# Kernel optimization log

Measured on AMD Instinct MI355X. Metric: run time of the kernel, lower is better.

The kernel has to match this reference:

```python
import jax, jax.numpy as jnp
import numpy as np

B, S, D, H = 4, 2048, 1024, 16
HD = D // H


def setup_inputs() -> dict:
    key = jax.random.key(0)
    ks = jax.random.split(key, 6)
    s = 1.0 / np.sqrt(D)
    return {
        "x": jax.random.normal(ks[0], (B, S, D), dtype=jnp.float32),
        "Wq": jax.random.normal(ks[1], (D, D), dtype=jnp.float32) * s,
        "Wk": jax.random.normal(ks[2], (D, D), dtype=jnp.float32) * s,
        "Wv": jax.random.normal(ks[3], (D, D), dtype=jnp.float32) * s,
        "Wo": jax.random.normal(ks[4], (D, D), dtype=jnp.float32) * s,
        "bo": jnp.zeros((D,), dtype=jnp.float32),
    }


def reference(x, Wq, Wk, Wv, Wo, bo):
    b, n, d = x.shape
    # QKV projections (torch Linear: x @ W.T, but weights here are stored as [d_in, d_out])
    q = (x @ Wq).reshape(b, n, H, HD).transpose(0, 2, 1, 3)  # [b,h,n,hd]
    k = (x @ Wk).reshape(b, n, H, HD).transpose(0, 2, 1, 3)
    v = (x @ Wv).reshape(b, n, H, HD).transpose(0, 2, 1, 3)
    scores = jnp.einsum("bhqd,bhkd->bhqk", q, k) / np.sqrt(HD)
    causal = jnp.tril(jnp.ones((n, n), dtype=bool))  # True = keep
    scores = jnp.where(causal, scores, -jnp.inf)
    attn = jax.nn.softmax(scores, axis=-1)
    ctx = jnp.einsum("bhqk,bhkd->bhqd", attn, v)
    ctx = ctx.transpose(0, 2, 1, 3).reshape(b, n, d)
    return ctx @ Wo + bo
```

## Files before the change

kernel.cpp:

```cpp
#include <hip/hip_runtime.h>
#include <hip/hip_bf16.h>

typedef __bf16 bf16;
typedef __bf16 bf16x4 __attribute__((ext_vector_type(4)));
typedef __bf16 bf16x8 __attribute__((ext_vector_type(8)));
typedef float f32x4 __attribute__((ext_vector_type(4)));

static constexpr int Bn = 4, Sn = 2048, Dn = 1024, Hn = 16, HDn = 64;
static constexpr int Mn = Bn * Sn;

__device__ __forceinline__ void gload_lds16(const void* g, void* l) {
  __builtin_amdgcn_global_load_lds(
      (const __attribute__((address_space(1))) unsigned int*)g,
      (__attribute__((address_space(3))) unsigned int*)l, 16, 0, 0);
}

__global__ void cvt_x_kernel(const float* __restrict__ x, bf16* __restrict__ xb, int n8) {
  int i = blockIdx.x * blockDim.x + threadIdx.x;
  if (i >= n8) return;
  const float4* p = reinterpret_cast<const float4*>(x) + (size_t)i * 2;
  float4 a = p[0], b = p[1];
  bf16x8 v;
  v[0] = (bf16)a.x; v[1] = (bf16)a.y; v[2] = (bf16)a.z; v[3] = (bf16)a.w;
  v[4] = (bf16)b.x; v[5] = (bf16)b.y; v[6] = (bf16)b.z; v[7] = (bf16)b.w;
  *(reinterpret_cast<bf16x8*>(xb) + i) = v;
}

struct alignas(8) B4 { bf16 e[4]; };

__global__ void transpose_w_kernel(const float* __restrict__ W0, const float* __restrict__ W1,
                                   const float* __restrict__ W2, const float* __restrict__ W3,
                                   bf16* __restrict__ WtQKV, bf16* __restrict__ Wot) {
  __shared__ bf16 tile[64][65];
  const int which = blockIdx.z;
  const float* W = (which == 0) ? W0 : (which == 1) ? W1 : (which == 2) ? W2 : W3;
  bf16* out = (which < 3) ? (WtQKV + (size_t)which * 1024 * 1024) : Wot;
  const int k0 = blockIdx.y * 64, n0 = blockIdx.x * 64;
  const int t = threadIdx.x;
  const int tr = t >> 4, tc = (t & 15) * 4;
#pragma unroll
  for (int rr = 0; rr < 4; ++rr) {
    const int row = rr * 16 + tr;
    float4 v = *reinterpret_cast<const float4*>(&W[(size_t)(k0 + row) * 1024 + n0 + tc]);
    tile[row][tc + 0] = (bf16)v.x; tile[row][tc + 1] = (bf16)v.y;
    tile[row][tc + 2] = (bf16)v.z; tile[row][tc + 3] = (bf16)v.w;
  }
  __syncthreads();
#pragma unroll
  for (int rr = 0; rr < 4; ++rr) {
    const int row = rr * 16 + tr;
    B4 o;
#pragma unroll
    for (int j = 0; j < 4; ++j) o.e[j] = tile[tc + j][row];
    *reinterpret_cast<B4*>(&out[(size_t)(n0 + row) * 1024 + k0 + tc]) = o;
  }
}

template <int MODE>
__global__ __launch_bounds__(256, 2)
void gemm_kernel(const bf16* __restrict__ A, const bf16* __restrict__ Bt,
                 float* __restrict__ Co, const float* __restrict__ bias,
                 bf16* __restrict__ Qo, bf16* __restrict__ Ko, bf16* __restrict__ Vto) {
  __shared__ bf16 Al[2][128 * 64];
  __shared__ bf16 Bl[2][128 * 64];
  const int tid = threadIdx.x;
  const int lane = tid & 63;
  const int wv = tid >> 6;
  const int wm = wv >> 1, wn = wv & 1;
  const int lr = lane & 15, lg = lane >> 4;
  const int m0 = blockIdx.y * 128, n0 = blockIdx.x * 128;

  int soff[4];
  const bf16* srcA[4];
  const bf16* srcB[4];
#pragma unroll
  for (int it = 0; it < 4; ++it) {
    const int elem = it * 2048 + tid * 8;
    const int row = elem >> 6;
    const int g = (elem >> 3) & 7;
    const int gs = g ^ (row & 7);
    soff[it] = elem;
    srcA[it] = A + (size_t)(m0 + row) * 1024 + gs * 8;
    srcB[it] = Bt + (size_t)(n0 + row) * 1024 + gs * 8;
  }

  f32x4 acc[4][4] = {};

#pragma unroll
  for (int it = 0; it < 4; ++it) {
    gload_lds16(srcA[it], (bf16*)&Al[0][0] + soff[it]);
    gload_lds16(srcB[it], (bf16*)&Bl[0][0] + soff[it]);
  }
  __syncthreads();

  for (int ks = 0; ks < 16; ++ks) {
    const int cur = ks & 1;
    if (ks + 1 < 16) {
      const int kn = (ks + 1) * 64;
#pragma unroll
      for (int it = 0; it < 4; ++it) {
        gload_lds16(srcA[it] + kn, (bf16*)&Al[cur ^ 1][0] + soff[it]);
        gload_lds16(srcB[it] + kn, (bf16*)&Bl[cur ^ 1][0] + soff[it]);
      }
    }
    const bf16* AlF = Al[cur];
    const bf16* BlF = Bl[cur];
#pragma unroll
    for (int kk = 0; kk < 2; ++kk) {
      bf16x8 af[4], bfr[4];
#pragma unroll
      for (int i = 0; i < 4; ++i) {
        const int row = wm * 64 + i * 16 + lr;
        af[i] = *reinterpret_cast<const bf16x8*>(AlF + row * 64 + (((kk * 4 + lg) ^ (row & 7)) << 3));
      }
#pragma unroll
      for (int i = 0; i < 4; ++i) {
        const int row = wn * 64 + i * 16 + lr;
        bfr[i] = *reinterpret_cast<const bf16x8*>(BlF + row * 64 + (((kk * 4 + lg) ^ (row & 7)) << 3));
      }
#pragma unroll
      for (int mi = 0; mi < 4; ++mi)
#pragma unroll
        for (int ni = 0; ni < 4; ++ni)
          acc[mi][ni] = __builtin_amdgcn_mfma_f32_16x16x32_bf16(af[mi], bfr[ni], acc[mi][ni], 0, 0, 0);
    }
    __syncthreads();
  }

  const int mrow = lg * 4;
  if (MODE == 0) {
    const int w = n0 >> 10;
    const int nl0 = n0 & 1023;
    if (w == 2) {
      const int b = m0 >> 11;
      const int s0 = (m0 & 2047) + wm * 64 + mrow;
#pragma unroll
      for (int ni = 0; ni < 4; ++ni) {
        const int nl = nl0 + wn * 64 + ni * 16 + lr;
        const int h = nl >> 6, hd = nl & 63;
        bf16* vbase = Vto + ((size_t)(b * 16 + h) * 64 + hd) * 2048;
#pragma unroll
        for (int mi = 0; mi < 4; ++mi) {
          B4 o;
#pragma unroll
          for (int i = 0; i < 4; ++i) o.e[i] = (bf16)acc[mi][ni][i];
          *reinterpret_cast<B4*>(&vbase[s0 + mi * 16]) = o;
        }
      }
    } else {
      const float fs = (w == 0) ? 0.18033688011112042f : 1.0f;
#pragma unroll
      for (int ni = 0; ni < 4; ++ni) {
        const int nl = nl0 + wn * 64 + ni * 16 + lr;
        const int h = nl >> 6, hd = nl & 63;
        bf16* dst = (w == 0) ? Qo : Ko;
#pragma unroll
        for (int mi = 0; mi < 4; ++mi) {
#pragma unroll
          for (int i = 0; i < 4; ++i) {
            const int m_g = m0 + wm * 64 + mi * 16 + mrow + i;
            const int b = m_g >> 11, s = m_g & 2047;
            dst[((size_t)(b * 16 + h) * 2048 + s) * 64 + hd] = (bf16)(acc[mi][ni][i] * fs);
          }
        }
      }
    }
  } else {
#pragma unroll
    for (int ni = 0; ni < 4; ++ni) {
      const int n_g = n0 + wn * 64 + ni * 16 + lr;
      const float bv = bias[n_g];
#pragma unroll
      for (int mi = 0; mi < 4; ++mi) {
#pragma unroll
        for (int i = 0; i < 4; ++i) {
          const int m_g = m0 + wm * 64 + mi * 16 + mrow + i;
          Co[(size_t)m_g * 1024 + n_g] = acc[mi][ni][i] + bv;
        }
      }
    }
  }
}

__device__ __forceinline__ unsigned int pack2(float lo, float hi) {
  union { bf16 bb[2]; unsigned int u; } c;
  c.bb[0] = (bf16)lo; c.bb[1] = (bf16)hi;
  return c.u;
}

__device__ __forceinline__ void attn_tile(const bf16* __restrict__ KlF,
                                          const bf16* __restrict__ VlF,
                                          const bf16x8 (&aq)[2], f32x4 (&acc)[4],
                                          float& lst, int kv0, int qrow, bool domask,
                                          int lr, int lg) {
  f32x4 sc[4] = {};
#pragma unroll
  for (int kk = 0; kk < 2; ++kk) {
    bf16x8 ak[4];
#pragma unroll
    for (int ni = 0; ni < 4; ++ni) {
      const int row = ni * 16 + lr;
      ak[ni] = *reinterpret_cast<const bf16x8*>(KlF + row * 64 + (((kk * 4 + lg) ^ (row & 7)) << 3));
    }
    __builtin_amdgcn_s_setprio(1);
#pragma unroll
    for (int ni = 0; ni < 4; ++ni)
      sc[ni] = __builtin_amdgcn_mfma_f32_16x16x32_bf16(ak[ni], aq[kk], sc[ni], 0, 0, 0);
    __builtin_amdgcn_s_setprio(0);
  }
  float p[4][4];
  float rs = 0.f;
#pragma unroll
  for (int ni = 0; ni < 4; ++ni)
#pragma unroll
    for (int r = 0; r < 4; ++r) {
      float pv = __builtin_amdgcn_exp2f(sc[ni][r]);
      if (domask && (kv0 + ni * 16 + lg * 4 + r > qrow)) pv = 0.f;
      p[ni][r] = pv;
      rs += pv;
    }
  rs += __shfl_xor(rs, 16);
  rs += __shfl_xor(rs, 32);
  lst += rs;
  unsigned int pk[4][2];
#pragma unroll
  for (int ni = 0; ni < 4; ++ni)
#pragma unroll
    for (int tt = 0; tt < 2; ++tt)
      pk[ni][tt] = pack2(p[ni][2 * tt], p[ni][2 * tt + 1]);
#pragma unroll
  for (int kk = 0; kk < 2; ++kk) {
    union { unsigned int u[4]; bf16x8 v; } ap;
#pragma unroll
    for (int w = 0; w < 4; ++w) ap.u[w] = pk[2 * kk + (w >> 1)][w & 1];
    const int g1 = 4 * kk + (lg >> 1), g2 = g1 + 2, off = 4 * (lg & 1);
#pragma unroll
    for (int ni = 0; ni < 4; ++ni) {
      const int row = ni * 16 + lr;
      union { bf16x4 q[2]; bf16x8 v; } av;
      av.q[0] = *reinterpret_cast<const bf16x4*>(VlF + row * 64 + ((g1 ^ (row & 7)) << 3) + off);
      av.q[1] = *reinterpret_cast<const bf16x4*>(VlF + row * 64 + ((g2 ^ (row & 7)) << 3) + off);
      __builtin_amdgcn_s_setprio(1);
      acc[ni] = __builtin_amdgcn_mfma_f32_16x16x32_bf16(av.v, ap.v, acc[ni], 0, 0, 0);
      __builtin_amdgcn_s_setprio(0);
    }
  }
}

__global__ __launch_bounds__(256, 4)
void attn_kernel(const bf16* __restrict__ Q, const bf16* __restrict__ K,
                 const bf16* __restrict__ Vt, bf16* __restrict__ ctx) {
  __shared__ bf16 Kl[2][4096];
  __shared__ bf16 Vl[2][4096];
  const int tid = threadIdx.x, lane = tid & 63, wv = tid >> 6;
  const int lr = lane & 15, lg = lane >> 4, lk = lg * 8;
  const int bh = blockIdx.y;
  const int pi = blockIdx.x;
  const bf16* Qh = Q + (size_t)bh * Sn * 64;
  const bf16* Kh = K + (size_t)bh * Sn * 64;
  const bf16* Vh = Vt + (size_t)bh * 64 * (size_t)Sn;
  const int b = bh >> 4, h = bh & 15;

  const int e0 = tid * 8, e1 = 2048 + tid * 8;
  const int r0 = e0 >> 6, r1 = e1 >> 6;
  const int gs0 = ((e0 >> 3) & 7) ^ (r0 & 7), gs1 = ((e1 >> 3) & 7) ^ (r1 & 7);
  const bf16* srcK0 = Kh + r0 * 64 + gs0 * 8;
  const bf16* srcK1 = Kh + r1 * 64 + gs1 * 8;
  const bf16* srcV0 = Vh + (size_t)r0 * Sn + gs0 * 8;
  const bf16* srcV1 = Vh + (size_t)r1 * Sn + gs1 * 8;

  const int tA = 31 - pi, tB = pi;
  const int qwA = tA * 64 + wv * 16, qwB = tB * 64 + wv * 16;
  const int qrowA = qwA + lr, qrowB = qwB + lr;

  bf16x8 aqA[2], aqB[2];
#pragma unroll
  for (int kk = 0; kk < 2; ++kk) {
    aqA[kk] = *reinterpret_cast<const bf16x8*>(&Qh[(size_t)(qwA + lr) * 64 + kk * 32 + lk]);
    aqB[kk] = *reinterpret_cast<const bf16x8*>(&Qh[(size_t)(qwB + lr) * 64 + kk * 32 + lk]);
  }

  f32x4 accA[4] = {}, accB[4] = {};
  float lstA = 0.f, lstB = 0.f;

  gload_lds16(srcK0, &Kl[0][e0]);
  gload_lds16(srcK1, &Kl[0][e1]);
  gload_lds16(srcV0, &Vl[0][e0]);
  gload_lds16(srcV1, &Vl[0][e1]);
  __syncthreads();

  for (int t = 0; t <= tA; ++t) {
    const int cur = t & 1;
    if (t < tA) {
      const int kvn = (t + 1) * 64;
      gload_lds16(srcK0 + kvn * 64, &Kl[cur ^ 1][e0]);
      gload_lds16(srcK1 + kvn * 64, &Kl[cur ^ 1][e1]);
      gload_lds16(srcV0 + kvn, &Vl[cur ^ 1][e0]);
      gload_lds16(srcV1 + kvn, &Vl[cur ^ 1][e1]);
    }
    const bf16* KlF = Kl[cur];
    const bf16* VlF = Vl[cur];
    attn_tile(KlF, VlF, aqA, accA, lstA, t * 64, qrowA, t == tA, lr, lg);
    if (t <= tB)
      attn_tile(KlF, VlF, aqB, accB, lstB, t * 64, qrowB, t == tB, lr, lg);
    __syncthreads();
  }

  {
    const float inv = 1.f / lstA;
    bf16* cbase = ctx + (((size_t)b * Sn + qwA + lr) * 16 + h) * 64;
#pragma unroll
    for (int ni = 0; ni < 4; ++ni) {
      B4 o;
#pragma unroll
      for (int r = 0; r < 4; ++r) o.e[r] = (bf16)(accA[ni][r] * inv);
      *reinterpret_cast<B4*>(cbase + ni * 16 + lg * 4) = o;
    }
  }
  {
    const float inv = 1.f / lstB;
    bf16* cbase = ctx + (((size_t)b * Sn + qwB + lr) * 16 + h) * 64;
#pragma unroll
    for (int ni = 0; ni < 4; ++ni) {
      B4 o;
#pragma unroll
      for (int r = 0; r < 4; ++r) o.e[r] = (bf16)(accB[ni][r] * inv);
      *reinterpret_cast<B4*>(cbase + ni * 16 + lg * 4) = o;
    }
  }
}

extern "C" void kernel_launch(void* const* d_in, const int* in_sizes, int n_in,
                              void* d_out, int out_size, void* d_ws, size_t ws_size,
                              hipStream_t stream) {
  const float* x = (const float*)d_in[0];
  const float* Wq = (const float*)d_in[1];
  const float* Wk = (const float*)d_in[2];
  const float* Wv = (const float*)d_in[3];
  const float* Wo = (const float*)d_in[4];
  const float* bo = (const float*)d_in[5];

  char* ws = (char*)d_ws;
  bf16* xb    = (bf16*)(ws);
  bf16* WtQKV = (bf16*)(ws + 0x1000000);
  bf16* Wot   = (bf16*)(ws + 0x1600000);
  bf16* Qb    = (bf16*)(ws + 0x1800000);
  bf16* Kb    = (bf16*)(ws + 0x2800000);
  bf16* Vtb   = (bf16*)(ws + 0x3800000);
  bf16* ctx   = xb;

  cvt_x_kernel<<<dim3(Mn * Dn / 8 / 256), dim3(256), 0, stream>>>(x, xb, Mn * Dn / 8);
  transpose_w_kernel<<<dim3(16, 16, 4), dim3(256), 0, stream>>>(Wq, Wk, Wv, Wo, WtQKV, Wot);
  gemm_kernel<0><<<dim3(24, 64), dim3(256), 0, stream>>>(xb, WtQKV, nullptr, nullptr, Qb, Kb, Vtb);
  attn_kernel<<<dim3(16, 64), dim3(256), 0, stream>>>(Qb, Kb, Vtb, ctx);
  gemm_kernel<1><<<dim3(8, 64), dim3(256), 0, stream>>>(ctx, Wot, (float*)d_out, bo,
                                                        nullptr, nullptr, nullptr);
}
```

Baseline: 174.3 us.

## Share K/V fragment loads across both query tiles and permute V^T layout

The attention loop now loads the K and V fragments from LDS once per KV tile and reuses them for both query tiles (A and B), where before each attn_tile call reloaded them. The V^T store in the projection kernel uses a permuted sequence order so that each V fragment can be read with a single 16-byte LDS load instead of two 8-byte loads. The goal is fewer LDS reads and better MFMA issue density. In exchange the kernel holds more fragments in registers, and launch bounds drop from 4 to 3 waves, which lowers occupancy.

```diff
diff --git a/kernel.cpp b/kernel.cpp
--- a/kernel.cpp
+++ b/kernel.cpp
@@ -133,7 +133,7 @@
     const int nl0 = n0 & 1023;
     if (w == 2) {
       const int b = m0 >> 11;
-      const int s0 = (m0 & 2047) + wm * 64 + mrow;
+      const int sBase = (m0 & 2047) + wm * 64 + lg * 8;
 #pragma unroll
       for (int ni = 0; ni < 4; ++ni) {
         const int nl = nl0 + wn * 64 + ni * 16 + lr;
@@ -144,7 +144,8 @@
           B4 o;
 #pragma unroll
           for (int i = 0; i < 4; ++i) o.e[i] = (bf16)acc[mi][ni][i];
-          *reinterpret_cast<B4*>(&vbase[s0 + mi * 16]) = o;
+          const int sNew = sBase + ((mi >> 1) << 5) + ((mi & 1) << 2);
+          *reinterpret_cast<B4*>(&vbase[sNew]) = o;
         }
       }
     } else {
@@ -188,26 +189,8 @@
   return c.u;
 }
 
-__device__ __forceinline__ void attn_tile(const bf16* __restrict__ KlF,
-                                          const bf16* __restrict__ VlF,
-                                          const bf16x8 (&aq)[2], f32x4 (&acc)[4],
-                                          float& lst, int kv0, int qrow, bool domask,
-                                          int lr, int lg) {
-  f32x4 sc[4] = {};
-#pragma unroll
-  for (int kk = 0; kk < 2; ++kk) {
-    bf16x8 ak[4];
-#pragma unroll
-    for (int ni = 0; ni < 4; ++ni) {
-      const int row = ni * 16 + lr;
-      ak[ni] = *reinterpret_cast<const bf16x8*>(KlF + row * 64 + (((kk * 4 + lg) ^ (row & 7)) << 3));
-    }
-    __builtin_amdgcn_s_setprio(1);
-#pragma unroll
-    for (int ni = 0; ni < 4; ++ni)
-      sc[ni] = __builtin_amdgcn_mfma_f32_16x16x32_bf16(ak[ni], aq[kk], sc[ni], 0, 0, 0);
-    __builtin_amdgcn_s_setprio(0);
-  }
+__device__ __forceinline__ float smax_pack(const f32x4 (&sc)[4], unsigned int (&pk)[4][2],
+                                           int kv0, int qrow, bool domask, int lg) {
   float p[4][4];
   float rs = 0.f;
 #pragma unroll
@@ -219,35 +202,15 @@
       p[ni][r] = pv;
       rs += pv;
     }
-  rs += __shfl_xor(rs, 16);
-  rs += __shfl_xor(rs, 32);
-  lst += rs;
-  unsigned int pk[4][2];
 #pragma unroll
   for (int ni = 0; ni < 4; ++ni)
 #pragma unroll
     for (int tt = 0; tt < 2; ++tt)
       pk[ni][tt] = pack2(p[ni][2 * tt], p[ni][2 * tt + 1]);
-#pragma unroll
-  for (int kk = 0; kk < 2; ++kk) {
-    union { unsigned int u[4]; bf16x8 v; } ap;
-#pragma unroll
-    for (int w = 0; w < 4; ++w) ap.u[w] = pk[2 * kk + (w >> 1)][w & 1];
-    const int g1 = 4 * kk + (lg >> 1), g2 = g1 + 2, off = 4 * (lg & 1);
-#pragma unroll
-    for (int ni = 0; ni < 4; ++ni) {
-      const int row = ni * 16 + lr;
-      union { bf16x4 q[2]; bf16x8 v; } av;
-      av.q[0] = *reinterpret_cast<const bf16x4*>(VlF + row * 64 + ((g1 ^ (row & 7)) << 3) + off);
-      av.q[1] = *reinterpret_cast<const bf16x4*>(VlF + row * 64 + ((g2 ^ (row & 7)) << 3) + off);
-      __builtin_amdgcn_s_setprio(1);
-      acc[ni] = __builtin_amdgcn_mfma_f32_16x16x32_bf16(av.v, ap.v, acc[ni], 0, 0, 0);
-      __builtin_amdgcn_s_setprio(0);
-    }
-  }
-}
-
-__global__ __launch_bounds__(256, 4)
+  return rs;
+}
+
+__global__ __launch_bounds__(256, 3)
 void attn_kernel(const bf16* __restrict__ Q, const bf16* __restrict__ K,
                  const bf16* __restrict__ Vt, bf16* __restrict__ ctx) {
   __shared__ bf16 Kl[2][4096];
@@ -298,11 +261,82 @@
       gload_lds16(srcV0 + kvn, &Vl[cur ^ 1][e0]);
       gload_lds16(srcV1 + kvn, &Vl[cur ^ 1][e1]);
     }
+    const int kv0 = t * 64;
     const bf16* KlF = Kl[cur];
     const bf16* VlF = Vl[cur];
-    attn_tile(KlF, VlF, aqA, accA, lstA, t * 64, qrowA, t == tA, lr, lg);
-    if (t <= tB)
-      attn_tile(KlF, VlF, aqB, accB, lstB, t * 64, qrowB, t == tB, lr, lg);
+    const bool actB = (t <= tB);
+
+    bf16x8 ak[2][4];
+#pragma unroll
+    for (int kk = 0; kk < 2; ++kk)
+#pragma unroll
+      for (int ni = 0; ni < 4; ++ni) {
+        const int row = ni * 16 + lr;
+        ak[kk][ni] = *reinterpret_cast<const bf16x8*>(KlF + row * 64 + (((kk * 4 + lg) ^ (row & 7)) << 3));
+      }
+    f32x4 scA[4] = {};
+    __builtin_amdgcn_s_setprio(1);
+#pragma unroll
+    for (int kk = 0; kk < 2; ++kk)
+#pragma unroll
+      for (int ni = 0; ni < 4; ++ni)
+        scA[ni] = __builtin_amdgcn_mfma_f32_16x16x32_bf16(ak[kk][ni], aqA[kk], scA[ni], 0, 0, 0);
+    __builtin_amdgcn_s_setprio(0);
+    unsigned int pkA[4][2] = {};
+    {
+      float rs = smax_pack(scA, pkA, kv0, qrowA, t == tA, lg);
+      rs += __shfl_xor(rs, 16);
+      rs += __shfl_xor(rs, 32);
+      lstA += rs;
+    }
+    unsigned int pkB[4][2] = {};
+    if (actB) {
+      f32x4 scB[4] = {};
+      __builtin_amdgcn_s_setprio(1);
+#pragma unroll
+      for (int kk = 0; kk < 2; ++kk)
+#pragma unroll
+        for (int ni = 0; ni < 4; ++ni)
+          scB[ni] = __builtin_amdgcn_mfma_f32_16x16x32_bf16(ak[kk][ni], aqB[kk], scB[ni], 0, 0, 0);
+      __builtin_amdgcn_s_setprio(0);
+      float rs = smax_pack(scB, pkB, kv0, qrowB, t == tB, lg);
+      rs += __shfl_xor(rs, 16);
+      rs += __shfl_xor(rs, 32);
+      lstB += rs;
+    }
+
+    bf16x8 av[2][4];
+#pragma unroll
+    for (int kk = 0; kk < 2; ++kk)
+#pragma unroll
+      for (int ni = 0; ni < 4; ++ni) {
+        const int row = ni * 16 + lr;
+        av[kk][ni] = *reinterpret_cast<const bf16x8*>(VlF + row * 64 + (((kk * 4 + lg) ^ (row & 7)) << 3));
+      }
+    __builtin_amdgcn_s_setprio(1);
+#pragma unroll
+    for (int kk = 0; kk < 2; ++kk) {
+      union { unsigned int u[4]; bf16x8 v; } ap;
+#pragma unroll
+      for (int w = 0; w < 4; ++w) ap.u[w] = pkA[2 * kk + (w >> 1)][w & 1];
+#pragma unroll
+      for (int ni = 0; ni < 4; ++ni)
+        accA[ni] = __builtin_amdgcn_mfma_f32_16x16x32_bf16(av[kk][ni], ap.v, accA[ni], 0, 0, 0);
+    }
+    __builtin_amdgcn_s_setprio(0);
+    if (actB) {
+      __builtin_amdgcn_s_setprio(1);
+#pragma unroll
+      for (int kk = 0; kk < 2; ++kk) {
+        union { unsigned int u[4]; bf16x8 v; } ap;
+#pragma unroll
+        for (int w = 0; w < 4; ++w) ap.u[w] = pkB[2 * kk + (w >> 1)][w & 1];
+#pragma unroll
+        for (int ni = 0; ni < 4; ++ni)
+          accB[ni] = __builtin_amdgcn_mfma_f32_16x16x32_bf16(av[kk][ni], ap.v, accB[ni], 0, 0, 0);
+      }
+      __builtin_amdgcn_s_setprio(0);
+    }
     __syncthreads();
   }
 
```

Result: no change. 175.6 us (+0.8%).
